# Kernel optimization log

Hardware: AMD Instinct MI355X
Metric: run time of the kernel (lower is better)

The kernel has to match this reference:

```python
import jax, jax.numpy as jnp
import numpy as np

N_NODES = 100000


def setup_inputs() -> dict:
    key = jax.random.key(0)
    k1, k2, k3, k4, k5, k6 = jax.random.split(key, 6)
    x = jax.random.normal(k1, (N_NODES, 6), dtype=jnp.float32)
    edge_index = jax.random.randint(k2, (2, 6400000), 0, N_NODES, dtype=jnp.int64)
    # PointCloudGNN.lin: Linear(6, 64); PointCloudModel.lin: Linear(64, 3)
    W1 = jax.random.normal(k3, (64, 6), dtype=jnp.float32) * (1.0 / np.sqrt(6))
    b1 = jax.random.normal(k4, (64,), dtype=jnp.float32) * 0.01
    W2 = jax.random.normal(k5, (3, 64), dtype=jnp.float32) * (1.0 / np.sqrt(64))
    b2 = jax.random.normal(k6, (3,), dtype=jnp.float32) * 0.01
    return {"x": x, "edge_index": edge_index, "W1": W1, "b1": b1, "W2": W2, "b2": b2}


def reference(x, edge_index, W1, b1, W2, b2):
    n = x.shape[0]
    # add_self_loops: append (i, i) for every node
    loops = jnp.arange(n, dtype=edge_index.dtype)
    row = jnp.concatenate([edge_index[0], loops])  # source nodes (j)
    col = jnp.concatenate([edge_index[1], loops])  # target nodes (i)
    # linear transform: [N, 6] -> [N, 64]
    h = x @ W1.T + b1
    # degree computed over row (as in the source), self-loops guarantee deg >= 1
    deg = jax.ops.segment_sum(jnp.ones_like(row, dtype=h.dtype), row, num_segments=n)
    deg_inv_sqrt = deg ** -0.5
    norm = deg_inv_sqrt[row] * deg_inv_sqrt[col]  # [E+N]
    # message: norm * x_j (x_j = h[row]); aggregate (add) at col
    msg = norm[:, None] * h[row]  # [E+N, 64]
    agg = jax.ops.segment_sum(msg, col, num_segments=n)  # [N, 64]
    out = jax.nn.relu(agg) @ W2.T + b2  # [N, 3]
    return out
```

## Files before the change

kernel.cpp:

```cpp
#include <hip/hip_runtime.h>

#define NTHREADS 256
#define SD     128
#define NMAX   102400
#define BAGG   256
#define APAD   9
#define LBITS  8
#define SA     2
#define MAXBIN 512
#define CHUNK  8192

#define QSCALE 2097152.0f
#define QINV   (1.0f / 2097152.0f)
#define FSCALE 4096.0f
#define FINV   (1.0f / 4096.0f)

__global__ __launch_bounds__(1024)
void k_deg(const int* __restrict__ row, int E, int n,
           unsigned char* __restrict__ degPart) {
    __shared__ unsigned int h[NMAX / 4];
    for (int i = threadIdx.x; i < NMAX / 4; i += blockDim.x) h[i] = 0u;
    __syncthreads();

    const int s = blockIdx.x;
    const int E4 = E >> 2;
    const int c4 = (E4 + SD - 1) / SD;
    const int s4 = s * c4;
    const int e4 = min(s4 + c4, E4);
    const int4* row4 = (const int4*)row;
    for (int t = s4 + threadIdx.x; t < e4; t += blockDim.x) {
        int4 r = row4[t];
        atomicAdd(&h[r.x >> 2], 1u << ((r.x & 3) << 3));
        atomicAdd(&h[r.y >> 2], 1u << ((r.y & 3) << 3));
        atomicAdd(&h[r.z >> 2], 1u << ((r.z & 3) << 3));
        atomicAdd(&h[r.w >> 2], 1u << ((r.w & 3) << 3));
    }
    if (s == SD - 1 && threadIdx.x == 0) {
        for (int e = E & ~3; e < E; ++e) {
            int v = row[e];
            atomicAdd(&h[v >> 2], 1u << ((v & 3) << 3));
        }
    }
    __syncthreads();

    unsigned int* gp = (unsigned int*)degPart;
    const int nw = n >> 2;
    for (int i = threadIdx.x; i < nw; i += blockDim.x)
        gp[(size_t)s * nw + i] = h[i];
}

__global__ void k_disy(const unsigned char* __restrict__ degPart,
                       const float* __restrict__ x, int n,
                       float* __restrict__ dis, int* __restrict__ yq) {
    const int nw = n >> 2;
    int p = blockIdx.x * blockDim.x + threadIdx.x;
    if (p >= nw) return;
    const unsigned int* gp = (const unsigned int*)degPart;
    unsigned s0 = 0, s1 = 0, s2 = 0, s3 = 0;
    for (int s = 0; s < SD; ++s) {
        unsigned w = gp[(size_t)s * nw + p];
        s0 += w & 255u;
        s1 += (w >> 8) & 255u;
        s2 += (w >> 16) & 255u;
        s3 += w >> 24;
    }
    unsigned ss[4] = {s0, s1, s2, s3};
    const float2* x2 = (const float2*)x;
    const int i0 = p * 4;
    #pragma unroll
    for (int k = 0; k < 4; ++k) {
        int i = i0 + k;
        float d = rsqrtf((float)ss[k] + 1.0f);
        dis[i] = d;
        float2 a = x2[3 * i + 0], b = x2[3 * i + 1], c = x2[3 * i + 2];
        float fs = d * FSCALE;
        float vals[6] = {fs * a.x, fs * a.y, fs * b.x, fs * b.y, fs * c.x, fs * c.y};
        int q[6];
        #pragma unroll
        for (int m = 0; m < 6; ++m)
            q[m] = __float2int_rn(fminf(fmaxf(vals[m], -32767.0f), 32767.0f));
        int4* q4 = (int4*)(yq + (size_t)i * 4);
        q4[0] = make_int4((q[0] & 0xffff) | (q[1] << 16),
                          (q[2] & 0xffff) | (q[3] << 16),
                          (q[4] & 0xffff) | (q[5] << 16),
                          __float2int_rn(d * QSCALE));
    }
}

__global__ __launch_bounds__(1024)
void k_bin(const int* __restrict__ col, const int* __restrict__ row,
           int E, int cap, unsigned int* __restrict__ bins,
           int* __restrict__ binCursor) {
    __shared__ int cnt[MAXBIN];
    __shared__ int lofs[MAXBIN];
    __shared__ int base[MAXBIN];
    __shared__ int cur[MAXBIN];
    __shared__ unsigned int ent[CHUNK];
    __shared__ unsigned short ebin[CHUNK];

    for (int i = threadIdx.x; i < MAXBIN; i += blockDim.x) { cnt[i] = 0; cur[i] = 0; }
    __syncthreads();

    const int E4 = E >> 2;
    const int s4 = blockIdx.x * (CHUNK / 4);
    const int e4 = min(s4 + CHUNK / 4, E4);
    const int4* col4 = (const int4*)col;
    const int4* row4 = (const int4*)row;

    for (int t = s4 + threadIdx.x; t < e4; t += blockDim.x) {
        int4 c = col4[t];
        atomicAdd(&cnt[c.x >> LBITS], 1);
        atomicAdd(&cnt[c.y >> LBITS], 1);
        atomicAdd(&cnt[c.z >> LBITS], 1);
        atomicAdd(&cnt[c.w >> LBITS], 1);
    }
    __syncthreads();

    if (threadIdx.x < MAXBIN) lofs[threadIdx.x] = cnt[threadIdx.x];
    __syncthreads();
    for (int d = 1; d < MAXBIN; d <<= 1) {
        int v = 0;
        if (threadIdx.x >= d && threadIdx.x < MAXBIN) v = lofs[threadIdx.x - d];
        __syncthreads();
        if (threadIdx.x >= d && threadIdx.x < MAXBIN) lofs[threadIdx.x] += v;
        __syncthreads();
    }
    if (threadIdx.x < MAXBIN) {
        lofs[threadIdx.x] -= cnt[threadIdx.x];
        if (cnt[threadIdx.x] > 0)
            base[threadIdx.x] = atomicAdd(&binCursor[threadIdx.x], cnt[threadIdx.x]);
    }
    __syncthreads();

    for (int t = s4 + threadIdx.x; t < e4; t += blockDim.x) {
        int4 c = col4[t];
        int4 r = row4[t];
        int b, p;
        b = c.x >> LBITS; p = lofs[b] + atomicAdd(&cur[b], 1);
        ent[p] = (unsigned)(c.x & (BAGG - 1)) | ((unsigned)r.x << LBITS);
        ebin[p] = (unsigned short)b;
        b = c.y >> LBITS; p = lofs[b] + atomicAdd(&cur[b], 1);
        ent[p] = (unsigned)(c.y & (BAGG - 1)) | ((unsigned)r.y << LBITS);
        ebin[p] = (unsigned short)b;
        b = c.z >> LBITS; p = lofs[b] + atomicAdd(&cur[b], 1);
        ent[p] = (unsigned)(c.z & (BAGG - 1)) | ((unsigned)r.z << LBITS);
        ebin[p] = (unsigned short)b;
        b = c.w >> LBITS; p = lofs[b] + atomicAdd(&cur[b], 1);
        ent[p] = (unsigned)(c.w & (BAGG - 1)) | ((unsigned)r.w << LBITS);
        ebin[p] = (unsigned short)b;
    }
    __syncthreads();

    const int total = (e4 - s4) * 4;
    for (int i = threadIdx.x; i < total; i += blockDim.x) {
        int b = ebin[i];
        int dst = base[b] + (i - lofs[b]);
        if (dst < cap) bins[(size_t)b * cap + dst] = ent[i];
    }
}

__global__ __launch_bounds__(256)
void k_agg2(const unsigned int* __restrict__ bins, const int* __restrict__ binCursor,
            const int* __restrict__ yq, float* __restrict__ aggPart,
            int n, int cap) {
    __shared__ int acc[BAGG * APAD];
    const int b = blockIdx.x / SA;
    const int s = blockIdx.x % SA;
    const int lo = b * BAGG;

    for (int i = threadIdx.x; i < BAGG * APAD; i += blockDim.x) acc[i] = 0;
    __syncthreads();

    int cnt = binCursor[b];
    if (cnt > cap) cnt = cap;
    const int chunk = (((cnt + SA - 1) / SA) + 3) & ~3;
    const int st = min(s * chunk, cnt);
    const int en = min(st + chunk, cnt);
    const int len = en - st;
    const int len4 = len >> 2;
    const unsigned int* bp = bins + (size_t)b * cap;
    const uint4* bp4 = (const uint4*)(bp + st);
    const int4* y4 = (const int4*)yq;

    #define ACCUM(lv, pk)                                                  \
        {                                                                  \
            int* qq = acc + (lv) * APAD;                                   \
            atomicAdd(qq + 0, (int)(short)((pk).x & 0xffff));              \
            atomicAdd(qq + 1, (pk).x >> 16);                               \
            atomicAdd(qq + 2, (int)(short)((pk).y & 0xffff));              \
            atomicAdd(qq + 3, (pk).y >> 16);                               \
            atomicAdd(qq + 4, (int)(short)((pk).z & 0xffff));              \
            atomicAdd(qq + 5, (pk).z >> 16);                               \
            atomicAdd(qq + 6, (pk).w);                                     \
        }

    for (int q = threadIdx.x; q < len4; q += blockDim.x) {
        uint4 v = bp4[q];
        unsigned l0 = v.x & (BAGG - 1u); int j0 = (int)(v.x >> LBITS);
        unsigned l1 = v.y & (BAGG - 1u); int j1 = (int)(v.y >> LBITS);
        unsigned l2 = v.z & (BAGG - 1u); int j2 = (int)(v.z >> LBITS);
        unsigned l3 = v.w & (BAGG - 1u); int j3 = (int)(v.w >> LBITS);
        int4 p0 = y4[j0];
        int4 p1 = y4[j1];
        int4 p2 = y4[j2];
        int4 p3 = y4[j3];
        ACCUM(l0, p0)
        ACCUM(l1, p1)
        ACCUM(l2, p2)
        ACCUM(l3, p3)
    }
    for (int t = st + len4 * 4 + threadIdx.x; t < en; t += blockDim.x) {
        unsigned v = bp[t];
        unsigned l = v & (BAGG - 1u);
        int j = (int)(v >> LBITS);
        int4 pk = y4[j];
        ACCUM(l, pk)
    }
    #undef ACCUM
    __syncthreads();

    const int nb = min(BAGG, n - lo);
    for (int i = threadIdx.x; i < nb; i += blockDim.x) {
        const int* src = acc + (size_t)i * APAD;
        float4* op = (float4*)(aggPart + ((size_t)s * n + (lo + i)) * 8);
        op[0] = make_float4((float)src[0] * FINV, (float)src[1] * FINV,
                            (float)src[2] * FINV, (float)src[3] * FINV);
        op[1] = make_float4((float)src[4] * FINV, (float)src[5] * FINV,
                            (float)src[6] * QINV, 0.0f);
    }
}

__global__ void k_final_r(const float* __restrict__ x, const float* __restrict__ dis,
                          const float* __restrict__ aggPart,
                          const float* __restrict__ W1, const float* __restrict__ b1,
                          const float* __restrict__ W2, const float* __restrict__ b2,
                          float* __restrict__ out, int n) {
    __shared__ float sW1[64 * 6];
    __shared__ float sb1[64];
    __shared__ float sW2[3 * 64];
    __shared__ float sb2[3];
    for (int k = threadIdx.x; k < 64 * 6; k += blockDim.x) sW1[k] = W1[k];
    for (int k = threadIdx.x; k < 64; k += blockDim.x) sb1[k] = b1[k];
    for (int k = threadIdx.x; k < 3 * 64; k += blockDim.x) sW2[k] = W2[k];
    if (threadIdx.x < 3) sb2[threadIdx.x] = b2[threadIdx.x];
    __syncthreads();

    int i = blockIdx.x * blockDim.x + threadIdx.x;
    if (i >= n) return;

    float4 G0 = make_float4(0.f, 0.f, 0.f, 0.f);
    float4 G1 = make_float4(0.f, 0.f, 0.f, 0.f);
    for (int s = 0; s < SA; ++s) {
        const float4* pp = (const float4*)(aggPart + ((size_t)s * n + i) * 8);
        float4 a = pp[0], b = pp[1];
        G0.x += a.x; G0.y += a.y; G0.z += a.z; G0.w += a.w;
        G1.x += b.x; G1.y += b.y; G1.z += b.z;
    }

    float di = dis[i];
    const float2* x2 = (const float2*)x;
    float2 xa = x2[3 * i + 0], xb = x2[3 * i + 1], xc = x2[3 * i + 2];

    float ax[6];
    ax[0] = di * (G0.x + di * xa.x);
    ax[1] = di * (G0.y + di * xa.y);
    ax[2] = di * (G0.z + di * xb.x);
    ax[3] = di * (G0.w + di * xb.y);
    ax[4] = di * (G1.x + di * xc.x);
    ax[5] = di * (G1.y + di * xc.y);
    float s = di * (G1.z + di);

    float o0 = sb2[0], o1 = sb2[1], o2 = sb2[2];
    for (int f = 0; f < 64; ++f) {
        float v = s * sb1[f];
        #pragma unroll
        for (int k = 0; k < 6; ++k) v = fmaf(ax[k], sW1[f * 6 + k], v);
        v = fmaxf(v, 0.0f);
        o0 = fmaf(v, sW2[0 * 64 + f], o0);
        o1 = fmaf(v, sW2[1 * 64 + f], o1);
        o2 = fmaf(v, sW2[2 * 64 + f], o2);
    }
    out[(size_t)i * 3 + 0] = o0;
    out[(size_t)i * 3 + 1] = o1;
    out[(size_t)i * 3 + 2] = o2;
}

__global__ void k_count1(const int* __restrict__ idx, int E, int* __restrict__ cnt) {
    int t = blockIdx.x * blockDim.x + threadIdx.x;
    int e = t * 4;
    if (e + 3 < E) {
        int4 r = ((const int4*)idx)[t];
        atomicAdd(&cnt[r.x], 1); atomicAdd(&cnt[r.y], 1);
        atomicAdd(&cnt[r.z], 1); atomicAdd(&cnt[r.w], 1);
    } else if (e < E) {
        for (int q = e; q < E; ++q) atomicAdd(&cnt[idx[q]], 1);
    }
}
__global__ void k_dis(const int* __restrict__ cnt, float* __restrict__ dis, int n) {
    int t = blockIdx.x * blockDim.x + threadIdx.x;
    if (t < n) dis[t] = rsqrtf((float)cnt[t] + 1.0f);
}
__global__ void k_scatter(const int* __restrict__ row, const int* __restrict__ col,
                          const float* __restrict__ x, const float* __restrict__ dis,
                          float* __restrict__ agg, int E) {
    int e = blockIdx.x * blockDim.x + threadIdx.x;
    if (e >= E) return;
    int j = row[e];
    int i = col[e];
    float w = dis[j];
    const float2* x2 = (const float2*)x;
    float2 a = x2[3 * j + 0], b = x2[3 * j + 1], c = x2[3 * j + 2];
    float* p = agg + (size_t)i * 8;
    atomicAdd(p + 0, w * a.x); atomicAdd(p + 1, w * a.y);
    atomicAdd(p + 2, w * b.x); atomicAdd(p + 3, w * b.y);
    atomicAdd(p + 4, w * c.x); atomicAdd(p + 5, w * c.y);
    atomicAdd(p + 6, w);
}
__global__ void k_final(const float* __restrict__ x, const float* __restrict__ dis,
                        const float* __restrict__ agg,
                        const float* __restrict__ W1, const float* __restrict__ b1,
                        const float* __restrict__ W2, const float* __restrict__ b2,
                        float* __restrict__ out, int n) {
    __shared__ float sW1[64 * 6];
    __shared__ float sb1[64];
    __shared__ float sW2[3 * 64];
    __shared__ float sb2[3];
    for (int k = threadIdx.x; k < 64 * 6; k += blockDim.x) sW1[k] = W1[k];
    for (int k = threadIdx.x; k < 64; k += blockDim.x) sb1[k] = b1[k];
    for (int k = threadIdx.x; k < 3 * 64; k += blockDim.x) sW2[k] = W2[k];
    if (threadIdx.x < 3) sb2[threadIdx.x] = b2[threadIdx.x];
    __syncthreads();
    int i = blockIdx.x * blockDim.x + threadIdx.x;
    if (i >= n) return;
    float di = dis[i];
    const float4* ag4 = (const float4*)(agg + (size_t)i * 8);
    float4 g0 = ag4[0], g1 = ag4[1];
    const float2* x2 = (const float2*)x;
    float2 xa = x2[3 * i + 0], xb = x2[3 * i + 1], xc = x2[3 * i + 2];
    float ax[6];
    ax[0] = di * (g0.x + di * xa.x);
    ax[1] = di * (g0.y + di * xa.y);
    ax[2] = di * (g0.z + di * xb.x);
    ax[3] = di * (g0.w + di * xb.y);
    ax[4] = di * (g1.x + di * xc.x);
    ax[5] = di * (g1.y + di * xc.y);
    float s = di * (g1.z + di);
    float o0 = sb2[0], o1 = sb2[1], o2 = sb2[2];
    for (int f = 0; f < 64; ++f) {
        float v = s * sb1[f];
        #pragma unroll
        for (int k = 0; k < 6; ++k) v = fmaf(ax[k], sW1[f * 6 + k], v);
        v = fmaxf(v, 0.0f);
        o0 = fmaf(v, sW2[0 * 64 + f], o0);
        o1 = fmaf(v, sW2[1 * 64 + f], o1);
        o2 = fmaf(v, sW2[2 * 64 + f], o2);
    }
    out[(size_t)i * 3 + 0] = o0;
    out[(size_t)i * 3 + 1] = o1;
    out[(size_t)i * 3 + 2] = o2;
}

extern "C" void kernel_launch(void* const* d_in, const int* in_sizes, int n_in,
                              void* d_out, int out_size, void* d_ws, size_t ws_size,
                              hipStream_t stream) {
    const float* x  = (const float*)d_in[0];
    const int*   ei = (const int*)d_in[1];
    const float* W1 = (const float*)d_in[2];
    const float* b1 = (const float*)d_in[3];
    const float* W2 = (const float*)d_in[4];
    const float* b2 = (const float*)d_in[5];
    float* out = (float*)d_out;

    const int n = in_sizes[0] / 6;
    const int E = in_sizes[1] / 2;
    const int* row = ei;
    const int* col = ei + E;

    auto align1k = [](size_t v) { return (v + 1023) & ~(size_t)1023; };

    const int nbin = (n + BAGG - 1) / BAGG;
    const int cap  = ((E / nbin) + 1024 + 3) & ~3;

    size_t curOff  = 0;
    size_t regAOff = align1k(curOff + MAXBIN * 4);
    size_t regABytes = (size_t)SD * n;
    size_t binsBytes = (size_t)nbin * cap * 4;
    if (binsBytes > regABytes) regABytes = binsBytes;
    size_t aggOff  = align1k(regAOff + regABytes);
    size_t yOff    = align1k(aggOff + (size_t)SA * n * 8 * 4);
    size_t disOff  = align1k(yOff + (size_t)n * 4 * 4);
    size_t needed  = disOff + (size_t)n * 4;

    char* ws = (char*)d_ws;
    const bool okMain = ((E & 3) == 0) && ((n & 3) == 0) && (n <= NMAX) &&
                        (n <= (1 << 17)) && (nbin <= MAXBIN) && (ws_size >= needed);

    if (okMain) {
        int* binCursor            = (int*)(ws + curOff);
        unsigned char* degPart    = (unsigned char*)(ws + regAOff);
        unsigned int* bins        = (unsigned int*)(ws + regAOff);
        float* aggPart            = (float*)(ws + aggOff);
        int*   yq                 = (int*)(ws + yOff);
        float* dis                = (float*)(ws + disOff);

        hipMemsetAsync(binCursor, 0, MAXBIN * 4, stream);

        k_deg<<<SD, 1024, 0, stream>>>(row, E, n, degPart);

        int nw = n >> 2;
        k_disy<<<(nw + NTHREADS - 1) / NTHREADS, NTHREADS, 0, stream>>>(degPart, x, n, dis, yq);

        int nbBlocks = (E + CHUNK - 1) / CHUNK;
        k_bin<<<nbBlocks, 1024, 0, stream>>>(col, row, E, cap, bins, binCursor);

        k_agg2<<<nbin * SA, 256, 0, stream>>>(bins, binCursor, yq, aggPart, n, cap);

        int blocksN = (n + NTHREADS - 1) / NTHREADS;
        k_final_r<<<blocksN, NTHREADS, 0, stream>>>(x, dis, aggPart, W1, b1, W2, b2, out, n);
    } else {
        size_t fDisOff = align1k((size_t)n * 4);
        size_t fAggOff = align1k(fDisOff + (size_t)n * 4);
        int*   fCnt = (int*)ws;
        float* fDis = (float*)(ws + fDisOff);
        float* fAgg = (float*)(ws + fAggOff);

        hipMemsetAsync(ws, 0, fAggOff + (size_t)n * 8 * 4, stream);
        int threads4 = (E + 3) / 4;
        int blocksE4 = (threads4 + NTHREADS - 1) / NTHREADS;
        int blocksN  = (n + NTHREADS - 1) / NTHREADS;
        k_count1<<<blocksE4, NTHREADS, 0, stream>>>(row, E, fCnt);
        k_dis<<<blocksN, NTHREADS, 0, stream>>>(fCnt, fDis, n);
        int blocksE = (E + NTHREADS - 1) / NTHREADS;
        k_scatter<<<blocksE, NTHREADS, 0, stream>>>(row, col, x, fDis, fAgg, E);
        k_final<<<blocksN, NTHREADS, 0, stream>>>(x, fDis, fAgg, W1, b1, W2, b2, out, n);
    }
}
```

Before: 109.0 us.

## Merge aggregation splits with global integer atomics and drop the memset launch

Aggregation split blocks now atomically add their fixed-point integer accumulators into a single global buffer instead of writing per-split float partials that the final kernel sums. That buffer is zeroed inside the degree/scale kernel, and the bin cursor is zeroed inside the degree kernel, which removes the separate memset. The split count per bin doubles to raise parallelism in the aggregation stage. The cost is extra global atomics and possible integer overflow with more accumulation into one int. The tail loop for E not divisible by 4 is removed, which is safe only because the main path already requires E%4==0.

```diff
diff --git a/kernel.cpp b/kernel.cpp
--- a/kernel.cpp
+++ b/kernel.cpp
@@ -6,7 +6,7 @@
 #define BAGG   256
 #define APAD   9
 #define LBITS  8
-#define SA     2
+#define SA     4
 #define MAXBIN 512
 #define CHUNK  8192
 
@@ -17,7 +17,9 @@
 
 __global__ __launch_bounds__(1024)
 void k_deg(const int* __restrict__ row, int E, int n,
-           unsigned char* __restrict__ degPart) {
+           unsigned char* __restrict__ degPart, int* __restrict__ binCursor) {
+    if (blockIdx.x == 0 && threadIdx.x < MAXBIN) binCursor[threadIdx.x] = 0;
+
     __shared__ unsigned int h[NMAX / 4];
     for (int i = threadIdx.x; i < NMAX / 4; i += blockDim.x) h[i] = 0u;
     __syncthreads();
@@ -35,12 +37,6 @@
         atomicAdd(&h[r.z >> 2], 1u << ((r.z & 3) << 3));
         atomicAdd(&h[r.w >> 2], 1u << ((r.w & 3) << 3));
     }
-    if (s == SD - 1 && threadIdx.x == 0) {
-        for (int e = E & ~3; e < E; ++e) {
-            int v = row[e];
-            atomicAdd(&h[v >> 2], 1u << ((v & 3) << 3));
-        }
-    }
     __syncthreads();
 
     unsigned int* gp = (unsigned int*)degPart;
@@ -51,7 +47,8 @@
 
 __global__ void k_disy(const unsigned char* __restrict__ degPart,
                        const float* __restrict__ x, int n,
-                       float* __restrict__ dis, int* __restrict__ yq) {
+                       float* __restrict__ dis, int* __restrict__ yq,
+                       int* __restrict__ aggQ) {
     const int nw = n >> 2;
     int p = blockIdx.x * blockDim.x + threadIdx.x;
     if (p >= nw) return;
@@ -67,6 +64,12 @@
     unsigned ss[4] = {s0, s1, s2, s3};
     const float2* x2 = (const float2*)x;
     const int i0 = p * 4;
+
+    int4 z = make_int4(0, 0, 0, 0);
+    int4* az = (int4*)(aggQ + (size_t)i0 * 8);
+    #pragma unroll
+    for (int m = 0; m < 8; ++m) az[m] = z;
+
     #pragma unroll
     for (int k = 0; k < 4; ++k) {
         int i = i0 + k;
@@ -161,7 +164,7 @@
 
 __global__ __launch_bounds__(256)
 void k_agg2(const unsigned int* __restrict__ bins, const int* __restrict__ binCursor,
-            const int* __restrict__ yq, float* __restrict__ aggPart,
+            const int* __restrict__ yq, int* __restrict__ aggQ,
             int n, int cap) {
     __shared__ int acc[BAGG * APAD];
     const int b = blockIdx.x / SA;
@@ -222,16 +225,14 @@
     const int nb = min(BAGG, n - lo);
     for (int i = threadIdx.x; i < nb; i += blockDim.x) {
         const int* src = acc + (size_t)i * APAD;
-        float4* op = (float4*)(aggPart + ((size_t)s * n + (lo + i)) * 8);
-        op[0] = make_float4((float)src[0] * FINV, (float)src[1] * FINV,
-                            (float)src[2] * FINV, (float)src[3] * FINV);
-        op[1] = make_float4((float)src[4] * FINV, (float)src[5] * FINV,
-                            (float)src[6] * QINV, 0.0f);
+        int* dst = aggQ + (size_t)(lo + i) * 8;
+        #pragma unroll
+        for (int m = 0; m < 7; ++m) atomicAdd(dst + m, src[m]);
     }
 }
 
 __global__ void k_final_r(const float* __restrict__ x, const float* __restrict__ dis,
-                          const float* __restrict__ aggPart,
+                          const int* __restrict__ aggQ,
                           const float* __restrict__ W1, const float* __restrict__ b1,
                           const float* __restrict__ W2, const float* __restrict__ b2,
                           float* __restrict__ out, int n) {
@@ -248,27 +249,21 @@
     int i = blockIdx.x * blockDim.x + threadIdx.x;
     if (i >= n) return;
 
-    float4 G0 = make_float4(0.f, 0.f, 0.f, 0.f);
-    float4 G1 = make_float4(0.f, 0.f, 0.f, 0.f);
-    for (int s = 0; s < SA; ++s) {
-        const float4* pp = (const float4*)(aggPart + ((size_t)s * n + i) * 8);
-        float4 a = pp[0], b = pp[1];
-        G0.x += a.x; G0.y += a.y; G0.z += a.z; G0.w += a.w;
-        G1.x += b.x; G1.y += b.y; G1.z += b.z;
-    }
+    const int4* ag4 = (const int4*)(aggQ + (size_t)i * 8);
+    int4 g0 = ag4[0], g1 = ag4[1];
 
     float di = dis[i];
     const float2* x2 = (const float2*)x;
     float2 xa = x2[3 * i + 0], xb = x2[3 * i + 1], xc = x2[3 * i + 2];
 
     float ax[6];
-    ax[0] = di * (G0.x + di * xa.x);
-    ax[1] = di * (G0.y + di * xa.y);
-    ax[2] = di * (G0.z + di * xb.x);
-    ax[3] = di * (G0.w + di * xb.y);
-    ax[4] = di * (G1.x + di * xc.x);
-    ax[5] = di * (G1.y + di * xc.y);
-    float s = di * (G1.z + di);
+    ax[0] = di * ((float)g0.x * FINV + di * xa.x);
+    ax[1] = di * ((float)g0.y * FINV + di * xa.y);
+    ax[2] = di * ((float)g0.z * FINV + di * xb.x);
+    ax[3] = di * ((float)g0.w * FINV + di * xb.y);
+    ax[4] = di * ((float)g1.x * FINV + di * xc.x);
+    ax[5] = di * ((float)g1.y * FINV + di * xc.y);
+    float s = di * ((float)g1.z * QINV + di);
 
     float o0 = sb2[0], o1 = sb2[1], o2 = sb2[2];
     for (int f = 0; f < 64; ++f) {
@@ -387,7 +382,7 @@
     size_t binsBytes = (size_t)nbin * cap * 4;
     if (binsBytes > regABytes) regABytes = binsBytes;
     size_t aggOff  = align1k(regAOff + regABytes);
-    size_t yOff    = align1k(aggOff + (size_t)SA * n * 8 * 4);
+    size_t yOff    = align1k(aggOff + (size_t)n * 8 * 4);
     size_t disOff  = align1k(yOff + (size_t)n * 4 * 4);
     size_t needed  = disOff + (size_t)n * 4;
 
@@ -399,24 +394,22 @@
         int* binCursor            = (int*)(ws + curOff);
         unsigned char* degPart    = (unsigned char*)(ws + regAOff);
         unsigned int* bins        = (unsigned int*)(ws + regAOff);
-        float* aggPart            = (float*)(ws + aggOff);
+        int*   aggQ               = (int*)(ws + aggOff);
         int*   yq                 = (int*)(ws + yOff);
         float* dis                = (float*)(ws + disOff);
 
-        hipMemsetAsync(binCursor, 0, MAXBIN * 4, stream);
-
-        k_deg<<<SD, 1024, 0, stream>>>(row, E, n, degPart);
+        k_deg<<<SD, 1024, 0, stream>>>(row, E, n, degPart, binCursor);
 
         int nw = n >> 2;
-        k_disy<<<(nw + NTHREADS - 1) / NTHREADS, NTHREADS, 0, stream>>>(degPart, x, n, dis, yq);
+        k_disy<<<(nw + NTHREADS - 1) / NTHREADS, NTHREADS, 0, stream>>>(degPart, x, n, dis, yq, aggQ);
 
         int nbBlocks = (E + CHUNK - 1) / CHUNK;
         k_bin<<<nbBlocks, 1024, 0, stream>>>(col, row, E, cap, bins, binCursor);
 
-        k_agg2<<<nbin * SA, 256, 0, stream>>>(bins, binCursor, yq, aggPart, n, cap);
+        k_agg2<<<nbin * SA, 256, 0, stream>>>(bins, binCursor, yq, aggQ, n, cap);
 
         int blocksN = (n + NTHREADS - 1) / NTHREADS;
-        k_final_r<<<blocksN, NTHREADS, 0, stream>>>(x, dis, aggPart, W1, b1, W2, b2, out, n);
+        k_final_r<<<blocksN, NTHREADS, 0, stream>>>(x, dis, aggQ, W1, b1, W2, b2, out, n);
     } else {
         size_t fDisOff = align1k((size_t)n * 4);
         size_t fAggOff = align1k(fDisOff + (size_t)n * 4);
```

Result: slower. 140.5 us (+28.9%).
